# Performance work log

Hardware: AMD Instinct MI355X
Metric: run time of the kernel (lower is better)

Reference implementation:

```python
import jax, jax.numpy as jnp
import numpy as np

N_E = 16384
E_DIM = 64
BETA = 0.25


def setup_inputs() -> dict:
    key = jax.random.key(0)
    k1, k2 = jax.random.split(key)
    z = jax.random.normal(k1, (8, E_DIM, 32, 32), dtype=jnp.float32)
    # original inits uniform(-1/n_e, 1/n_e); use same scale
    emb_w = jax.random.uniform(k2, (N_E, E_DIM), dtype=jnp.float32,
                               minval=-1.0 / N_E, maxval=1.0 / N_E)
    return {"z": z, "emb_w": emb_w}


def reference(z, emb_w):
    # b c h w -> b h w c
    zp = jnp.transpose(z, (0, 2, 3, 1))              # [B,H,W,C]
    zf = zp.reshape(-1, E_DIM)                       # [N, e_dim]

    # pairwise squared distances: ||z||^2 + ||e||^2 - 2 z e^T
    d = (jnp.sum(zf * zf, axis=1, keepdims=True)
         + jnp.sum(emb_w * emb_w, axis=1)
         - 2.0 * jnp.einsum('nd,kd->nk', zf, emb_w))  # [N, n_e]
    idx = jnp.argmin(d, axis=1)                      # [N] int

    # usage tracking (codebook_usage starts at zeros each fresh module)
    usage = jnp.zeros((N_E,), dtype=jnp.float32).at[idx].max(1.0)
    num_unique = jnp.sum(usage).astype(jnp.int32)
    total_usage = jnp.sum(usage) / N_E

    z_q = emb_w[idx].reshape(zp.shape)               # [B,H,W,C]

    # legacy loss: ||sg(z_q)-z||^2 + beta*||z_q-sg(z)||^2
    loss = (jnp.mean((jax.lax.stop_gradient(z_q) - zp) ** 2)
            + BETA * jnp.mean((z_q - jax.lax.stop_gradient(zp)) ** 2))

    # straight-through estimator
    z_q = zp + jax.lax.stop_gradient(z_q - zp)
    z_q = jnp.transpose(z_q, (0, 3, 1, 2))           # b h w c -> b c h w

    return (z_q, loss, idx, num_unique, usage, total_usage)
```

## Files before the change

kernel.cpp:

```cpp
#include <hip/hip_runtime.h>
#include <math.h>

#define N_ROWS 8192
#define N_E    16384
#define EDIM   64
#define KSPLIT 16
#define KPER   1024
#define CHUNK  64
#define NCH    (KPER/CHUNK)

#define OFF_ZQ    0
#define OFF_LOSS  524288
#define OFF_IDX   524289
#define OFF_NUNIQ 532481
#define OFF_USAGE 532482
#define OFF_TOTAL 548866

typedef __attribute__((ext_vector_type(8)))  short  short8;
typedef __attribute__((ext_vector_type(8)))  ushort ushort8;
typedef __attribute__((ext_vector_type(4)))  float  f32x4;

__device__ ushort g_eh[N_E * EDIM];
__device__ ushort g_zh[N_ROWS * EDIM];
__device__ float  g_zt[N_ROWS * EDIM];

__device__ __forceinline__ ushort bf16hi(float v) {
    unsigned u = __float_as_uint(v);
    return (ushort)((u + 0x7fffu + ((u >> 16) & 1u)) >> 16);
}

__global__ __launch_bounds__(256) void vq_split(
    const float* __restrict__ z, const float* __restrict__ emb,
    float* __restrict__ anorm, float* __restrict__ out)
{
    __shared__ float lds[64][129];
    int bid = blockIdx.x, t = threadIdx.x;
    if (bid < 1024) {
        int i = bid * 256 + t;
        float4 v = ((const float4*)emb)[i];
        ushort4 h;
        h.x = bf16hi(v.x); h.y = bf16hi(v.y);
        h.z = bf16hi(v.z); h.w = bf16hi(v.w);
        ((ushort4*)g_eh)[i] = h;
    } else if (bid < 1088) {
        int zb = bid - 1024;
        int b = zb >> 3, hw0 = (zb & 7) << 7;
        const float* zp = z + (size_t)b * 65536 + hw0;
        for (int i = 0; i < 32; i++) {
            int j = i * 256 + t;
            int d = j >> 7, hw = j & 127;
            lds[d][hw] = zp[d * 1024 + hw];
        }
        __syncthreads();
        for (int i = 0; i < 4; i++) {
            int task = i * 256 + t;
            int hw = task >> 3, oct = task & 7;
            ushort8 h8; float4 f0, f1;
            float* fp0 = (float*)&f0; float* fp1 = (float*)&f1;
#pragma unroll
            for (int q = 0; q < 8; q++) {
                float v = lds[oct * 8 + q][hw];
                ((ushort*)&h8)[q] = bf16hi(v);
                if (q < 4) fp0[q] = v; else fp1[q - 4] = v;
            }
            size_t ro = (size_t)(b * 1024 + hw0 + hw) * 64 + oct * 8;
            *(ushort8*)(g_zh + ro) = h8;
            *(float4*)(g_zt + ro) = f0;
            *(float4*)(g_zt + ro + 4) = f1;
        }
        if (t < 128) {
            double s = 0.0;
            for (int d = 0; d < 64; d++) {
                float v = lds[d][t];
                s += (double)(v * v);
            }
            anorm[b * 1024 + hw0 + t] = (float)s;
        }
    } else {
        int i = (bid - 1088) * 256 + t;
        out[OFF_USAGE + i] = 0.f;
    }
}

__global__ __launch_bounds__(256) void vq_mfma(const float* __restrict__ anorm,
                                               unsigned* __restrict__ pcand)
{
    __shared__ __align__(16) ushort ebuf[2][8][CHUNK][8];

    const int t = threadIdx.x;
    const int w = t >> 6, lane = t & 63;
    const int rb = blockIdx.x >> 4, split = blockIdx.x & 15;
    const int n0 = rb * 128;
    const int nw = n0 + w * 32;
    const int kbase = split * KPER;
    const int col = lane & 15, quad = lane >> 4;

    short8 ah[2][2];
#pragma unroll
    for (int rt = 0; rt < 2; rt++)
#pragma unroll
        for (int s = 0; s < 2; s++) {
            size_t off = (size_t)(nw + rt * 16 + col) * 64 + s * 32 + quad * 8;
            ah[rt][s] = *(const short8*)(g_zh + off);
        }

    float av[8];
#pragma unroll
    for (int rt = 0; rt < 2; rt++)
#pragma unroll
        for (int r = 0; r < 4; r++)
            av[rt * 4 + r] = anorm[nw + rt * 16 + quad * 4 + r];

    unsigned p1[8], p2[8];
#pragma unroll
    for (int s = 0; s < 8; s++) { p1[s] = 0xFFFFFFFFu; p2[s] = 0xFFFFFFFFu; }

    auto stage = [&](int dbuf, int code0) {
#pragma unroll
        for (int jj = 0; jj < 2; jj++) {
            int g = w * 2 + jj;
            const ushort* ga = g_eh + (size_t)(code0 + lane) * 64 + g * 8;
            __builtin_amdgcn_global_load_lds(
                (const __attribute__((address_space(1))) void*)ga,
                (__attribute__((address_space(3))) void*)&ebuf[dbuf][g][0][0],
                16, 0, 0);
        }
    };

    const f32x4 Z = {0.f, 0.f, 0.f, 0.f};
    stage(0, kbase);
    for (int ch = 0; ch < NCH; ch++) {
        int cur = ch & 1;
        if (ch + 1 < NCH) {
            stage(cur ^ 1, kbase + (ch + 1) * CHUNK);
            asm volatile("s_waitcnt vmcnt(2)" ::: "memory");
        } else {
            asm volatile("s_waitcnt vmcnt(0)" ::: "memory");
        }
        __builtin_amdgcn_s_barrier();
        asm volatile("" ::: "memory");
#pragma unroll
        for (int ct = 0; ct < 4; ct++) {
            int cn = ct * 16 + col;
            short8 bh0 = *(const short8*)&ebuf[cur][quad][cn][0];
            short8 bh1 = *(const short8*)&ebuf[cur][4 + quad][cn][0];
            f32x4 a0 = __builtin_amdgcn_mfma_f32_16x16x32_bf16(ah[0][0], bh0, Z, 0, 0, 0);
            f32x4 a1 = __builtin_amdgcn_mfma_f32_16x16x32_bf16(ah[1][0], bh0, Z, 0, 0, 0);
            a0 = __builtin_amdgcn_mfma_f32_16x16x32_bf16(ah[0][1], bh1, a0, 0, 0, 0);
            a1 = __builtin_amdgcn_mfma_f32_16x16x32_bf16(ah[1][1], bh1, a1, 0, 0, 0);

            unsigned slot = (unsigned)(ch * 4 + ct);
#pragma unroll
            for (int rt = 0; rt < 2; rt++)
#pragma unroll
                for (int r = 0; r < 4; r++) {
                    int s = rt * 4 + r;
                    float c = rt ? a1[r] : a0[r];
                    float dq = fmaf(-2.0f, c, av[s]);
                    unsigned e = (__float_as_uint(dq) << 6) | slot;
                    unsigned p2n;
                    asm("v_med3_u32 %0, %1, %2, %3"
                        : "=v"(p2n) : "v"(p1[s]), "v"(p2[s]), "v"(e));
                    p2[s] = p2n;
                    p1[s] = (p1[s] < e) ? p1[s] : e;
                }
        }
        __builtin_amdgcn_s_barrier();
        asm volatile("" ::: "memory");
    }

    unsigned* sc = (unsigned*)ebuf;
#pragma unroll
    for (int s = 0; s < 8; s++) {
        int rt = s >> 2, r = s & 3;
        int lr = w * 32 + rt * 16 + quad * 4 + r;
        unsigned av26 = __float_as_uint(av[s]) & 0x03FFFFFFu;
#pragma unroll
        for (int j = 0; j < 2; j++) {
            unsigned p = j ? p2[s] : p1[s];
            unsigned dq26 = p >> 6;
            int diff = ((int)((dq26 - av26) << 6)) >> 6;
            unsigned packed = ((unsigned)(diff + 32768) << 10)
                            | ((p & 63u) << 4) | (unsigned)col;
            sc[lr * 32 + ((col * 2 + j + lr * 2) & 31)] = packed;
        }
    }
    __syncthreads();
    if (t < 128) {
        unsigned b0 = ~0u, b1 = ~0u, b2 = ~0u, b3 = ~0u;
        for (int q = 0; q < 32; q++) {
            unsigned v = sc[t * 32 + ((q + 2 * t) & 31)];
            unsigned m0 = (b0 > v) ? b0 : v;  b0 = (b0 < v) ? b0 : v;
            unsigned m1 = (b1 > m0) ? b1 : m0; b1 = (b1 < m0) ? b1 : m0;
            unsigned m2 = (b2 > m1) ? b2 : m1; b2 = (b2 < m1) ? b2 : m1;
            b3 = (b3 < m2) ? b3 : m2;
        }
        size_t base = (size_t)(n0 + t) * (KSPLIT * 4) + split * 4;
        pcand[base + 0] = b0; pcand[base + 1] = b1;
        pcand[base + 2] = b2; pcand[base + 3] = b3;
    }
}

__device__ __forceinline__ double shfl_xor_d(double p, int m) {
    int2 u = __builtin_bit_cast(int2, p);
    u.x = __shfl_xor(u.x, m);
    u.y = __shfl_xor(u.y, m);
    return __builtin_bit_cast(double, u);
}
__device__ __forceinline__ unsigned long long shfl_xor_u64(unsigned long long p, int m) {
    int2 u = __builtin_bit_cast(int2, p);
    u.x = __shfl_xor(u.x, m);
    u.y = __shfl_xor(u.y, m);
    return __builtin_bit_cast(unsigned long long, u);
}

__global__ __launch_bounds__(256) void vq_refine(
    const float* __restrict__ emb, const float* __restrict__ anorm,
    const unsigned* __restrict__ pcand,
    float* __restrict__ out, float* __restrict__ lossp)
{
    __shared__ float zq_s[4][65];
    __shared__ float red[4];
    int t = threadIdx.x;
    int lane = t & 63;
    int wv = t >> 6;
    int n = blockIdx.x * 4 + wv;
    int li = lane & 15;
    int qd = lane >> 4;

    float4 zf = *(const float4*)(g_zt + (size_t)n * 64 + li * 4);
    double z0 = (double)zf.x, z1 = (double)zf.y;
    double z2 = (double)zf.z, z3 = (double)zf.w;

    float av = anorm[n];
    unsigned av_b = __float_as_uint(av);

    unsigned v = pcand[(size_t)n * 64 + lane];
    unsigned dqb = av_b + (v >> 10) - 32768u;
    float cd = __uint_as_float(dqb);
    int ck = (lane >> 2) * KPER + (int)((v >> 4) & 63u) * 16 + (int)(v & 15u);

    float mn = cd;
#pragma unroll
    for (int s = 1; s < 64; s <<= 1) mn = fminf(mn, __shfl_xor(mn, s));
    float margin = __uint_as_float(av_b & 0xFF800000u) * 0x1p-18f;
    unsigned long long msk = __ballot(cd <= mn + margin);

    unsigned long long bkey = ~0ull;
    while (msk) {
        int ls[4];
#pragma unroll
        for (int j = 0; j < 4; j++) {
            ls[j] = msk ? (__ffsll((unsigned long long)msk) - 1) : -1;
            if (msk) msk &= msk - 1;
        }
        int lsel = ls[qd];
        int lsafe = (lsel >= 0) ? lsel : 0;
        int kq = __shfl(ck, lsafe);
        int k = (lsel >= 0) ? kq : -1;
        double s = 0.0;
        if (k >= 0) {
            float4 ef = *(const float4*)(emb + (size_t)k * EDIM + li * 4);
            s = fma(z3, (double)ef.w,
                fma(z2, (double)ef.z,
                fma(z1, (double)ef.y, z0 * (double)ef.x)));
        }
        s += shfl_xor_d(s, 1);
        s += shfl_xor_d(s, 2);
        s += shfl_xor_d(s, 4);
        s += shfl_xor_d(s, 8);
        if (k >= 0) {
            float c32 = (float)s;
            float dq = av - 2.0f * c32;
            unsigned long long key =
                ((unsigned long long)__float_as_uint(dq) << 32) | (unsigned)k;
            bkey = (key < bkey) ? key : bkey;
        }
    }
#pragma unroll
    for (int m = 1; m < 64; m <<= 1) {
        unsigned long long o = shfl_xor_u64(bkey, m);
        bkey = (o < bkey) ? o : bkey;
    }
    int bk = (int)(unsigned)(bkey & 0xffffffffu);
    if (lane == 0) {
        out[OFF_IDX + n] = (float)bk;
        out[OFF_USAGE + bk] = 1.0f;
    }
    float zqv = emb[(size_t)bk * 64 + lane];
    zq_s[wv][lane] = zqv;
    float d = zqv - g_zt[(size_t)n * 64 + lane];
    float ls = d * d;
#pragma unroll
    for (int s = 1; s < 64; s <<= 1) ls += __shfl_xor(ls, s);
    if (lane == 0) red[wv] = ls;
    __syncthreads();
    {
        int nb = blockIdx.x * 4;
        int b = nb >> 10, hw0 = nb & 1023;
        int c = t >> 2, i = t & 3;
        out[OFF_ZQ + b * 65536 + c * 1024 + hw0 + i] = zq_s[i][c];
    }
    if (t == 0) lossp[blockIdx.x] = red[0] + red[1] + red[2] + red[3];
}

__global__ __launch_bounds__(256) void vq_finale(
    const float* __restrict__ lossp, float* __restrict__ out)
{
    __shared__ double redd[4];
    __shared__ float  redf[4];
    int t = threadIdx.x, lane = t & 63, wv = t >> 6;
    float s = 0.f;
    for (int i = 0; i < 64; i++) s += out[OFF_USAGE + t + i * 256];
#pragma unroll
    for (int m = 1; m < 64; m <<= 1) s += __shfl_xor(s, m);
    if (lane == 0) redf[wv] = s;
    double ds = 0.0;
    for (int i = 0; i < 8; i++) ds += (double)lossp[t + i * 256];
    ds += shfl_xor_d(ds, 1);  ds += shfl_xor_d(ds, 2);
    ds += shfl_xor_d(ds, 4);  ds += shfl_xor_d(ds, 8);
    ds += shfl_xor_d(ds, 16); ds += shfl_xor_d(ds, 32);
    if (lane == 0) redd[wv] = ds;
    __syncthreads();
    if (t == 0) {
        float cnt = redf[0] + redf[1] + redf[2] + redf[3];
        double total = redd[0] + redd[1] + redd[2] + redd[3];
        out[OFF_NUNIQ] = cnt;
        out[OFF_TOTAL] = cnt / 16384.0f;
        out[OFF_LOSS]  = (float)(total * 1.25 / 524288.0);
    }
}

extern "C" void kernel_launch(void* const* d_in, const int* in_sizes, int n_in,
                              void* d_out, int out_size, void* d_ws, size_t ws_size,
                              hipStream_t stream)
{
    const float* z   = (const float*)d_in[0];
    const float* emb = (const float*)d_in[1];
    float* out = (float*)d_out;
    char* ws = (char*)d_ws;

    float*    anorm = (float*)ws;
    unsigned* pcand = (unsigned*)(ws + 32768);
    float*    lossp = (float*)(ws + 32768 + 2097152);

    vq_split <<<1152, 256, 0, stream>>>(z, emb, anorm, out);
    vq_mfma  <<<(N_ROWS / 128) * KSPLIT, 256, 0, stream>>>(anorm, pcand);
    vq_refine<<<N_ROWS / 4, 256, 0, stream>>>(emb, anorm, pcand, out, lossp);
    vq_finale<<<1, 256, 0, stream>>>(lossp, out);
}
```

Measured before the change: 112.4 us.

## Double codebook split, keep top-2 per split, fuse finale into refine

Raises the codebook split from 16 to 32 slices of 512 entries, so the MFMA distance kernel launches twice as many blocks. Each split now keeps a top-2 rather than a top-4 candidate set, which shortens the per-row sort, and the packed candidate format changes to match. The separate single-block finale kernel is removed. Its work moves into refine through a float atomic loss accumulator and a last-block-done counter, which saves one kernel launch. In exchange, the float atomic sum makes the loss total order-dependent and the candidate set per split is smaller.

```diff
diff --git a/kernel.cpp b/kernel.cpp
--- a/kernel.cpp
+++ b/kernel.cpp
@@ -4,8 +4,8 @@
 #define N_ROWS 8192
 #define N_E    16384
 #define EDIM   64
-#define KSPLIT 16
-#define KPER   1024
+#define KSPLIT 32
+#define KPER   512
 #define CHUNK  64
 #define NCH    (KPER/CHUNK)
 
@@ -31,7 +31,8 @@
 
 __global__ __launch_bounds__(256) void vq_split(
     const float* __restrict__ z, const float* __restrict__ emb,
-    float* __restrict__ anorm, float* __restrict__ out)
+    float* __restrict__ anorm, float* __restrict__ out,
+    float* __restrict__ lossacc, unsigned* __restrict__ done)
 {
     __shared__ float lds[64][129];
     int bid = blockIdx.x, t = threadIdx.x;
@@ -79,6 +80,7 @@
     } else {
         int i = (bid - 1088) * 256 + t;
         out[OFF_USAGE + i] = 0.f;
+        if (bid == 1088 && t == 0) { *lossacc = 0.f; *done = 0u; }
     }
 }
 
@@ -89,7 +91,7 @@
 
     const int t = threadIdx.x;
     const int w = t >> 6, lane = t & 63;
-    const int rb = blockIdx.x >> 4, split = blockIdx.x & 15;
+    const int rb = blockIdx.x >> 5, split = blockIdx.x & 31;
     const int n0 = rb * 128;
     const int nw = n0 + w * 32;
     const int kbase = split * KPER;
@@ -180,24 +182,21 @@
             unsigned p = j ? p2[s] : p1[s];
             unsigned dq26 = p >> 6;
             int diff = ((int)((dq26 - av26) << 6)) >> 6;
-            unsigned packed = ((unsigned)(diff + 32768) << 10)
-                            | ((p & 63u) << 4) | (unsigned)col;
+            unsigned packed = ((unsigned)(diff + 32768) << 9)
+                            | ((p & 31u) << 4) | (unsigned)col;
             sc[lr * 32 + ((col * 2 + j + lr * 2) & 31)] = packed;
         }
     }
     __syncthreads();
     if (t < 128) {
-        unsigned b0 = ~0u, b1 = ~0u, b2 = ~0u, b3 = ~0u;
+        unsigned b0 = ~0u, b1 = ~0u;
         for (int q = 0; q < 32; q++) {
             unsigned v = sc[t * 32 + ((q + 2 * t) & 31)];
             unsigned m0 = (b0 > v) ? b0 : v;  b0 = (b0 < v) ? b0 : v;
-            unsigned m1 = (b1 > m0) ? b1 : m0; b1 = (b1 < m0) ? b1 : m0;
-            unsigned m2 = (b2 > m1) ? b2 : m1; b2 = (b2 < m1) ? b2 : m1;
-            b3 = (b3 < m2) ? b3 : m2;
-        }
-        size_t base = (size_t)(n0 + t) * (KSPLIT * 4) + split * 4;
+            b1 = (b1 < m0) ? b1 : m0;
+        }
+        size_t base = (size_t)(n0 + t) * 64 + split * 2;
         pcand[base + 0] = b0; pcand[base + 1] = b1;
-        pcand[base + 2] = b2; pcand[base + 3] = b3;
     }
 }
 
@@ -216,11 +215,12 @@
 
 __global__ __launch_bounds__(256) void vq_refine(
     const float* __restrict__ emb, const float* __restrict__ anorm,
-    const unsigned* __restrict__ pcand,
-    float* __restrict__ out, float* __restrict__ lossp)
+    const unsigned* __restrict__ pcand, float* __restrict__ out,
+    float* __restrict__ lossacc, unsigned* __restrict__ done)
 {
     __shared__ float zq_s[4][65];
     __shared__ float red[4];
+    __shared__ unsigned lastflag;
     int t = threadIdx.x;
     int lane = t & 63;
     int wv = t >> 6;
@@ -236,9 +236,9 @@
     unsigned av_b = __float_as_uint(av);
 
     unsigned v = pcand[(size_t)n * 64 + lane];
-    unsigned dqb = av_b + (v >> 10) - 32768u;
+    unsigned dqb = av_b + ((v >> 9) & 0xFFFFu) - 32768u;
     float cd = __uint_as_float(dqb);
-    int ck = (lane >> 2) * KPER + (int)((v >> 4) & 63u) * 16 + (int)(v & 15u);
+    int ck = (lane >> 1) * KPER + (int)((v >> 4) & 31u) * 16 + (int)(v & 15u);
 
     float mn = cd;
 #pragma unroll
@@ -301,33 +301,28 @@
         int c = t >> 2, i = t & 3;
         out[OFF_ZQ + b * 65536 + c * 1024 + hw0 + i] = zq_s[i][c];
     }
-    if (t == 0) lossp[blockIdx.x] = red[0] + red[1] + red[2] + red[3];
-}
-
-__global__ __launch_bounds__(256) void vq_finale(
-    const float* __restrict__ lossp, float* __restrict__ out)
-{
-    __shared__ double redd[4];
-    __shared__ float  redf[4];
-    int t = threadIdx.x, lane = t & 63, wv = t >> 6;
-    float s = 0.f;
-    for (int i = 0; i < 64; i++) s += out[OFF_USAGE + t + i * 256];
-#pragma unroll
-    for (int m = 1; m < 64; m <<= 1) s += __shfl_xor(s, m);
-    if (lane == 0) redf[wv] = s;
-    double ds = 0.0;
-    for (int i = 0; i < 8; i++) ds += (double)lossp[t + i * 256];
-    ds += shfl_xor_d(ds, 1);  ds += shfl_xor_d(ds, 2);
-    ds += shfl_xor_d(ds, 4);  ds += shfl_xor_d(ds, 8);
-    ds += shfl_xor_d(ds, 16); ds += shfl_xor_d(ds, 32);
-    if (lane == 0) redd[wv] = ds;
+    if (t == 0) {
+        atomicAdd(lossacc, red[0] + red[1] + red[2] + red[3]);
+        __threadfence();
+        unsigned old = atomicAdd(done, 1u);
+        lastflag = (old == 2047u) ? 1u : 0u;
+    }
     __syncthreads();
-    if (t == 0) {
-        float cnt = redf[0] + redf[1] + redf[2] + redf[3];
-        double total = redd[0] + redd[1] + redd[2] + redd[3];
-        out[OFF_NUNIQ] = cnt;
-        out[OFF_TOTAL] = cnt / 16384.0f;
-        out[OFF_LOSS]  = (float)(total * 1.25 / 524288.0);
+    if (lastflag) {
+        float s = 0.f;
+        for (int i = 0; i < 64; i++) s += out[OFF_USAGE + t + i * 256];
+#pragma unroll
+        for (int sh = 1; sh < 64; sh <<= 1) s += __shfl_xor(s, sh);
+        if (lane == 0) red[wv] = s;
+        __syncthreads();
+        if (t == 0) {
+            __threadfence();
+            float total = atomicAdd(lossacc, 0.0f);
+            float cnt = red[0] + red[1] + red[2] + red[3];
+            out[OFF_NUNIQ] = cnt;
+            out[OFF_TOTAL] = cnt / 16384.0f;
+            out[OFF_LOSS]  = total * 1.25f / 524288.0f;
+        }
     }
 }
 
@@ -340,12 +335,12 @@
     float* out = (float*)d_out;
     char* ws = (char*)d_ws;
 
-    float*    anorm = (float*)ws;
-    unsigned* pcand = (unsigned*)(ws + 32768);
-    float*    lossp = (float*)(ws + 32768 + 2097152);
-
-    vq_split <<<1152, 256, 0, stream>>>(z, emb, anorm, out);
+    float*    anorm   = (float*)ws;
+    unsigned* pcand   = (unsigned*)(ws + 32768);
+    float*    lossacc = (float*)(ws + 32768 + 2097152);
+    unsigned* done    = (unsigned*)(ws + 32768 + 2097152 + 4);
+
+    vq_split <<<1152, 256, 0, stream>>>(z, emb, anorm, out, lossacc, done);
     vq_mfma  <<<(N_ROWS / 128) * KSPLIT, 256, 0, stream>>>(anorm, pcand);
-    vq_refine<<<N_ROWS / 4, 256, 0, stream>>>(emb, anorm, pcand, out, lossp);
-    vq_finale<<<1, 256, 0, stream>>>(lossp, out);
-}
+    vq_refine<<<N_ROWS / 4, 256, 0, stream>>>(emb, anorm, pcand, out, lossacc, done);
+}
```

Result: slower. 172.5 us (+53.5%).
